# Kernel optimization log

Measured on AMD Instinct MI355X. Metric: run time of the kernel, lower is better.

The kernel has to match this reference:

```python
import jax, jax.numpy as jnp
import numpy as np

B, TX, TY, D, H = 8, 128, 128, 512, 512
LN_EPS = 1e-3  # keras LayerNormalization default epsilon


def setup_inputs() -> dict:
    key = jax.random.key(0)
    ks = jax.random.split(key, 6)
    scale = 1.0 / np.sqrt(D)
    return {
        "context": jax.random.normal(ks[0], (B, TX, D), jnp.float32),
        "x": jax.random.normal(ks[1], (B, TY, D), jnp.float32),
        "Wa": jax.random.normal(ks[2], (D, H), jnp.float32) * scale,
        "bWa": jnp.zeros((H,), jnp.float32),
        "Ua": jax.random.normal(ks[3], (D, H), jnp.float32) * scale,
        "bUa": jnp.zeros((H,), jnp.float32),
        "Va": jax.random.normal(ks[4], (H, 1), jnp.float32) * (1.0 / np.sqrt(H)),
        "bVa": jnp.zeros((1,), jnp.float32),
        "gamma": jnp.ones((D,), jnp.float32),
        "beta": jnp.zeros((D,), jnp.float32),
    }


def reference(context, x, Wa, bWa, Ua, bUa, Va, bVa, gamma, beta):
    # context: [B,Tx,D], x: [B,Ty,D]
    Wc = context @ Wa + bWa                      # [B,Tx,H]
    Ux = x @ Ua + bUa                            # [B,Ty,H]
    t = jnp.tanh(Wc[:, None, :, :] + Ux[:, :, None, :])  # [B,Ty,Tx,H]
    scores = jnp.einsum('btxh,h->btx', t, Va[:, 0]) + bVa[0]  # [B,Ty,Tx]
    attn = jax.nn.softmax(scores, axis=-1)
    cv = jnp.einsum('btx,bxd->btd', attn, context)  # [B,Ty,D]
    mean = jnp.mean(cv, axis=-1, keepdims=True)
    var = jnp.mean(jnp.square(cv - mean), axis=-1, keepdims=True)
    cv = (cv - mean) * jax.lax.rsqrt(var + LN_EPS) * gamma + beta
    return cv + x
```

## Files before the change

kernel.cpp:

```cpp
#include <hip/hip_runtime.h>


#define SCALE 2.8853900817779268f

typedef __attribute__((ext_vector_type(8))) short short8;
typedef float floatx4 __attribute__((ext_vector_type(4)));

__device__ __forceinline__ unsigned short f2bf(float f) {
  union { float f; unsigned u; } c{f};
  unsigned r = (c.u + 0x7FFFu + ((c.u >> 16) & 1u)) >> 16;
  return (unsigned short)r;
}

__global__ __launch_bounds__(256) void prep_transpose(
    const float* __restrict__ Wa, const float* __restrict__ Ua,
    unsigned short* __restrict__ WaT, unsigned short* __restrict__ UaT) {
  const int id = blockIdx.x;
  const float* __restrict__ W = (id & 64) ? Ua : Wa;
  unsigned short* __restrict__ WT = (id & 64) ? UaT : WaT;
  const int tile = id & 63;
  const int k0 = (tile >> 3) * 64;
  const int n0 = (tile & 7) * 64;
  __shared__ float tl[64][65];
  const int t = threadIdx.x;
  const int c = t & 63, r0 = t >> 6;
#pragma unroll
  for (int p = 0; p < 16; p++) {
    const int k = r0 + p * 4;
    tl[k][c] = W[(k0 + k) * 512 + n0 + c];
  }
  __syncthreads();
  const int nl = t >> 2, kc = (t & 3) * 16;
  unsigned short ov[16];
#pragma unroll
  for (int q = 0; q < 16; q++) ov[q] = f2bf(tl[kc + q][nl]);
  *(short8*)&WT[(size_t)(n0 + nl) * 512 + k0 + kc]     = *(short8*)&ov[0];
  *(short8*)&WT[(size_t)(n0 + nl) * 512 + k0 + kc + 8] = *(short8*)&ov[8];
}

__global__ __launch_bounds__(512) void gemm_mfma(
    const float* __restrict__ ctx, const float* __restrict__ xin,
    const unsigned short* __restrict__ WaT, const unsigned short* __restrict__ UaT,
    const float* __restrict__ bWa, const float* __restrict__ bUa,
    float* __restrict__ WcT, float* __restrict__ Ux) {
  const bool second = (blockIdx.z != 0);
  const float* __restrict__ A = second ? xin : ctx;
  const unsigned short* __restrict__ BT = second ? UaT : WaT;
  const int m0 = blockIdx.x * 64, n0 = blockIdx.y * 64;

  __shared__ __align__(16) unsigned short As[64 * 32];
  __shared__ __align__(16) unsigned short Bs[64 * 32];

  const int t = threadIdx.x;
  const bool isA = (t < 256);
  const int s = isA ? t : (t - 256);
  const int sl = s & 63, sub = s >> 6;
  const int rl = sub * 16 + (sl & 15);
  const int kl = (sl >> 4) * 8;

  const float* aptr = A + (size_t)(m0 + rl) * 512 + kl;
  const unsigned short* bptr = BT + (size_t)(n0 + rl) * 512 + kl;

  const int lane = t & 63, w = t >> 6;
  const int wrow = w & 1, wcol = w >> 1;

  floatx4 acc[2] = {};

  float4 a0, a1; short8 bv;
  if (isA) { a0 = *(const float4*)(aptr); a1 = *(const float4*)(aptr + 4); }
  else     { bv = *(const short8*)(bptr); }

  for (int kt = 0; kt < 512; kt += 32) {
    if (isA) {
      short8 av;
      av[0] = (short)f2bf(a0.x); av[1] = (short)f2bf(a0.y);
      av[2] = (short)f2bf(a0.z); av[3] = (short)f2bf(a0.w);
      av[4] = (short)f2bf(a1.x); av[5] = (short)f2bf(a1.y);
      av[6] = (short)f2bf(a1.z); av[7] = (short)f2bf(a1.w);
      ((short8*)As)[s] = av;
    } else {
      ((short8*)Bs)[s] = bv;
    }
    __syncthreads();
    if (kt + 32 < 512) {
      if (isA) {
        a0 = *(const float4*)(aptr + kt + 32);
        a1 = *(const float4*)(aptr + kt + 36);
      } else {
        bv = *(const short8*)(bptr + kt + 32);
      }
    }
    short8 af[2], bf;
    af[0] = ((const short8*)As)[(wrow * 2 + 0) * 64 + lane];
    af[1] = ((const short8*)As)[(wrow * 2 + 1) * 64 + lane];
    bf    = ((const short8*)Bs)[wcol * 64 + lane];
#pragma unroll
    for (int i = 0; i < 2; i++)
      acc[i] = __builtin_amdgcn_mfma_f32_16x16x32_bf16(af[i], bf, acc[i], 0, 0, 0);
    __syncthreads();
  }

  const int quad = lane >> 4;
  const int h = n0 + wcol * 16 + (lane & 15);
  if (!second) {
    const float bias = bWa[h] + bUa[h];
#pragma unroll
    for (int i = 0; i < 2; i++) {
      const int mg0 = m0 + (wrow * 2 + i) * 16 + quad * 4;
      const int b = mg0 >> 7, tx0 = mg0 & 127;
      float4 o;
      o.x = (acc[i][0] + bias) * SCALE;
      o.y = (acc[i][1] + bias) * SCALE;
      o.z = (acc[i][2] + bias) * SCALE;
      o.w = (acc[i][3] + bias) * SCALE;
      *(float4*)&WcT[(size_t)b * 65536 + (size_t)h * 128 + tx0] = o;
    }
  } else {
#pragma unroll
    for (int i = 0; i < 2; i++) {
      const int mg0 = m0 + (wrow * 2 + i) * 16 + quad * 4;
#pragma unroll
      for (int r = 0; r < 4; r++)
        Ux[(size_t)(mg0 + r) * 512 + h] = acc[i][r] * SCALE;
    }
  }
}

__global__ __launch_bounds__(512) void attn3(
    const float* __restrict__ WcT, const float* __restrict__ Ux,
    const float* __restrict__ ctx, const float* __restrict__ xin,
    const float* __restrict__ Va,
    const float* __restrict__ gamma, const float* __restrict__ beta,
    float* __restrict__ out) {
  const int b = blockIdx.y;
  const int ty0 = blockIdx.x * 2;
  const int t = threadIdx.x;
  const int lane = t & 63, wv = t >> 6;

  __shared__ __align__(8) float2 s_ux[512];
  __shared__ float s_va[512];
  __shared__ float s_part[8][128];
  __shared__ __align__(8) float2 s_at[128];
  __shared__ float s_red[2][2][8];
  __shared__ float s_mv[2][2];

  {
    const float* uxb = Ux + (size_t)(b * 128 + ty0) * 512;
    for (int i = t; i < 1024; i += 512) {
      const int r = i >> 9, h = i & 511;
      ((float*)&s_ux[h])[r] = uxb[i];
    }
    s_va[t] = Va[t];
  }
  __syncthreads();

  const int tx = t & 127, hq = t >> 7;
  {
    const float* wp = WcT + (size_t)b * 65536 + (size_t)hq * 128 * 128 + tx;
    float a0 = 0.f, a1 = 0.f;
#pragma unroll 4
    for (int hh = 0; hh < 128; hh++) {
      const float w = wp[(size_t)hh * 128];
      const float2 u = s_ux[hq * 128 + hh];
      const float va = s_va[hq * 128 + hh];
      a0 = fmaf(va, __builtin_amdgcn_rcpf(1.0f + __builtin_amdgcn_exp2f(w + u.x)), a0);
      a1 = fmaf(va, __builtin_amdgcn_rcpf(1.0f + __builtin_amdgcn_exp2f(w + u.y)), a1);
    }
    s_part[hq * 2 + 0][tx] = a0;
    s_part[hq * 2 + 1][tx] = a1;
  }
  __syncthreads();

  if (wv < 2) {
    const int r = wv;
    float sA = -2.0f * (s_part[r][lane] + s_part[2 + r][lane] +
                        s_part[4 + r][lane] + s_part[6 + r][lane]);
    float sB = -2.0f * (s_part[r][lane + 64] + s_part[2 + r][lane + 64] +
                        s_part[4 + r][lane + 64] + s_part[6 + r][lane + 64]);
    float m = fmaxf(sA, sB);
#pragma unroll
    for (int off = 32; off; off >>= 1) m = fmaxf(m, __shfl_xor(m, off));
    const float eA = __expf(sA - m);
    const float eB = __expf(sB - m);
    float sm = eA + eB;
#pragma unroll
    for (int off = 32; off; off >>= 1) sm += __shfl_xor(sm, off);
    const float inv = __builtin_amdgcn_rcpf(sm);
    ((float*)&s_at[lane])[r] = eA * inv;
    ((float*)&s_at[lane + 64])[r] = eB * inv;
  }
  __syncthreads();

  const int d = t;
  float cv0 = 0.f, cv1 = 0.f;
  {
    const float* cp = ctx + (size_t)b * 65536 + d;
#pragma unroll 4
    for (int x = 0; x < 128; x++) {
      const float c = cp[(size_t)x * 512];
      const float2 at = s_at[x];
      cv0 = fmaf(at.x, c, cv0);
      cv1 = fmaf(at.y, c, cv1);
    }
  }

#pragma unroll
  for (int r = 0; r < 2; r++) {
    const float v = r ? cv1 : cv0;
    float sm = v, q = v * v;
#pragma unroll
    for (int off = 32; off; off >>= 1) {
      sm += __shfl_xor(sm, off);
      q += __shfl_xor(q, off);
    }
    if (lane == 0) { s_red[r][0][wv] = sm; s_red[r][1][wv] = q; }
  }
  __syncthreads();
  if (t < 2) {
    float sm = 0.f, q = 0.f;
#pragma unroll
    for (int i = 0; i < 8; i++) { sm += s_red[t][0][i]; q += s_red[t][1][i]; }
    const float mean = sm * (1.0f / 512.0f);
    const float var = q * (1.0f / 512.0f) - mean * mean;
    s_mv[t][0] = mean;
    s_mv[t][1] = __builtin_amdgcn_rsqf(var + 1e-3f);
  }
  __syncthreads();

  const float g = gamma[d], bb = beta[d];
#pragma unroll
  for (int r = 0; r < 2; r++) {
    const int row = b * 128 + ty0 + r;
    const float v = r ? cv1 : cv0;
    const float xv = xin[(size_t)row * 512 + d];
    out[(size_t)row * 512 + d] = (v - s_mv[r][0]) * s_mv[r][1] * g + bb + xv;
  }
}

extern "C" void kernel_launch(void* const* d_in, const int* in_sizes, int n_in,
                              void* d_out, int out_size, void* d_ws, size_t ws_size,
                              hipStream_t stream) {
  const float* ctx   = (const float*)d_in[0];
  const float* xin   = (const float*)d_in[1];
  const float* Wa    = (const float*)d_in[2];
  const float* bWa   = (const float*)d_in[3];
  const float* Ua    = (const float*)d_in[4];
  const float* bUa   = (const float*)d_in[5];
  const float* Va    = (const float*)d_in[6];
  const float* gamma = (const float*)d_in[8];
  const float* beta  = (const float*)d_in[9];
  float* out = (float*)d_out;

  char* ws = (char*)d_ws;
  float* WcT = (float*)ws;
  float* Ux  = (float*)(ws + (2u << 20));
  unsigned short* WaT = (unsigned short*)(ws + (4u << 20));
  unsigned short* UaT = (unsigned short*)(ws + (4u << 20) + (512u << 10));

  prep_transpose<<<128, 256, 0, stream>>>(Wa, Ua, WaT, UaT);
  gemm_mfma<<<dim3(16, 8, 2), 512, 0, stream>>>(ctx, xin, WaT, UaT, bWa, bUa, WcT, Ux);
  attn3<<<dim3(64, 8), 512, 0, stream>>>(WcT, Ux, ctx, xin, Va, gamma, beta, out);
}
```

Before: 117.7 us.

## Fuse weight transpose into GEMM and process four query rows per attention block

The separate prep_transpose kernel is removed. The GEMM now loads fp32 weights directly with strided per-k reads, converts them to bf16 in registers, and uses a 64-wide k step per stage. The attention kernel moves to 1024-thread blocks that each handle four query rows, so every WcT and context load is reused across more rows. The cost is one fewer launch, traded against strided uncoalesced-ish weight loads, fewer blocks (256) for the attention kernel, and idle threads in the context-reduction phase.

```diff
diff --git a/kernel.cpp b/kernel.cpp
--- a/kernel.cpp
+++ b/kernel.cpp
@@ -12,102 +12,76 @@
   return (unsigned short)r;
 }
 
-__global__ __launch_bounds__(256) void prep_transpose(
+__global__ __launch_bounds__(512) void gemm_all(
+    const float* __restrict__ ctx, const float* __restrict__ xin,
     const float* __restrict__ Wa, const float* __restrict__ Ua,
-    unsigned short* __restrict__ WaT, unsigned short* __restrict__ UaT) {
-  const int id = blockIdx.x;
-  const float* __restrict__ W = (id & 64) ? Ua : Wa;
-  unsigned short* __restrict__ WT = (id & 64) ? UaT : WaT;
-  const int tile = id & 63;
-  const int k0 = (tile >> 3) * 64;
-  const int n0 = (tile & 7) * 64;
-  __shared__ float tl[64][65];
-  const int t = threadIdx.x;
-  const int c = t & 63, r0 = t >> 6;
-#pragma unroll
-  for (int p = 0; p < 16; p++) {
-    const int k = r0 + p * 4;
-    tl[k][c] = W[(k0 + k) * 512 + n0 + c];
-  }
-  __syncthreads();
-  const int nl = t >> 2, kc = (t & 3) * 16;
-  unsigned short ov[16];
-#pragma unroll
-  for (int q = 0; q < 16; q++) ov[q] = f2bf(tl[kc + q][nl]);
-  *(short8*)&WT[(size_t)(n0 + nl) * 512 + k0 + kc]     = *(short8*)&ov[0];
-  *(short8*)&WT[(size_t)(n0 + nl) * 512 + k0 + kc + 8] = *(short8*)&ov[8];
-}
-
-__global__ __launch_bounds__(512) void gemm_mfma(
-    const float* __restrict__ ctx, const float* __restrict__ xin,
-    const unsigned short* __restrict__ WaT, const unsigned short* __restrict__ UaT,
     const float* __restrict__ bWa, const float* __restrict__ bUa,
     float* __restrict__ WcT, float* __restrict__ Ux) {
   const bool second = (blockIdx.z != 0);
   const float* __restrict__ A = second ? xin : ctx;
-  const unsigned short* __restrict__ BT = second ? UaT : WaT;
+  const float* __restrict__ W = second ? Ua : Wa;
   const int m0 = blockIdx.x * 64, n0 = blockIdx.y * 64;
 
-  __shared__ __align__(16) unsigned short As[64 * 32];
-  __shared__ __align__(16) unsigned short Bs[64 * 32];
+  __shared__ __align__(16) unsigned short As[512 * 8];
+  __shared__ __align__(16) unsigned short Bs[512 * 8];
 
   const int t = threadIdx.x;
-  const bool isA = (t < 256);
-  const int s = isA ? t : (t - 256);
-  const int sl = s & 63, sub = s >> 6;
-  const int rl = sub * 16 + (sl & 15);
-  const int kl = (sl >> 4) * 8;
-
-  const float* aptr = A + (size_t)(m0 + rl) * 512 + kl;
-  const unsigned short* bptr = BT + (size_t)(n0 + rl) * 512 + kl;
-
-  const int lane = t & 63, w = t >> 6;
-  const int wrow = w & 1, wcol = w >> 1;
-
+  const int lane = t & 63, wv = t >> 6;
+
+  const int skst = t >> 8;
+  const int ssub = (t >> 6) & 3;
+  const int srow = ssub * 16 + (lane & 15);
+  const int sk   = skst * 32 + (lane >> 4) * 8;
+
+  const float* aptr = A + (size_t)(m0 + srow) * 512 + sk;
+  const float* wptr = W + (size_t)sk * 512 + n0 + srow;
+
+  const int wrow = wv & 3, wcol = wv >> 2;
   floatx4 acc[2] = {};
 
-  float4 a0, a1; short8 bv;
-  if (isA) { a0 = *(const float4*)(aptr); a1 = *(const float4*)(aptr + 4); }
-  else     { bv = *(const short8*)(bptr); }
-
-  for (int kt = 0; kt < 512; kt += 32) {
-    if (isA) {
-      short8 av;
-      av[0] = (short)f2bf(a0.x); av[1] = (short)f2bf(a0.y);
-      av[2] = (short)f2bf(a0.z); av[3] = (short)f2bf(a0.w);
-      av[4] = (short)f2bf(a1.x); av[5] = (short)f2bf(a1.y);
-      av[6] = (short)f2bf(a1.z); av[7] = (short)f2bf(a1.w);
-      ((short8*)As)[s] = av;
-    } else {
-      ((short8*)Bs)[s] = bv;
-    }
+  float4 a0 = *(const float4*)(aptr);
+  float4 a1 = *(const float4*)(aptr + 4);
+  float bw[8];
+#pragma unroll
+  for (int j = 0; j < 8; j++) bw[j] = wptr[(size_t)j * 512];
+
+  for (int kt = 0; kt < 512; kt += 64) {
+    short8 av, bv;
+    av[0] = (short)f2bf(a0.x); av[1] = (short)f2bf(a0.y);
+    av[2] = (short)f2bf(a0.z); av[3] = (short)f2bf(a0.w);
+    av[4] = (short)f2bf(a1.x); av[5] = (short)f2bf(a1.y);
+    av[6] = (short)f2bf(a1.z); av[7] = (short)f2bf(a1.w);
+#pragma unroll
+    for (int j = 0; j < 8; j++) bv[j] = (short)f2bf(bw[j]);
+    ((short8*)As)[t] = av;
+    ((short8*)Bs)[t] = bv;
     __syncthreads();
-    if (kt + 32 < 512) {
-      if (isA) {
-        a0 = *(const float4*)(aptr + kt + 32);
-        a1 = *(const float4*)(aptr + kt + 36);
-      } else {
-        bv = *(const short8*)(bptr + kt + 32);
-      }
-    }
-    short8 af[2], bf;
-    af[0] = ((const short8*)As)[(wrow * 2 + 0) * 64 + lane];
-    af[1] = ((const short8*)As)[(wrow * 2 + 1) * 64 + lane];
-    bf    = ((const short8*)Bs)[wcol * 64 + lane];
-#pragma unroll
-    for (int i = 0; i < 2; i++)
-      acc[i] = __builtin_amdgcn_mfma_f32_16x16x32_bf16(af[i], bf, acc[i], 0, 0, 0);
+    if (kt + 64 < 512) {
+      a0 = *(const float4*)(aptr + kt + 64);
+      a1 = *(const float4*)(aptr + kt + 68);
+      const float* wp2 = wptr + (size_t)(kt + 64) * 512;
+#pragma unroll
+      for (int j = 0; j < 8; j++) bw[j] = wp2[(size_t)j * 512];
+    }
+#pragma unroll
+    for (int ks = 0; ks < 2; ks++) {
+      const short8 af  = ((const short8*)As)[ks * 256 + wrow * 64 + lane];
+      const short8 bf0 = ((const short8*)Bs)[ks * 256 + (wcol * 2 + 0) * 64 + lane];
+      const short8 bf1 = ((const short8*)Bs)[ks * 256 + (wcol * 2 + 1) * 64 + lane];
+      acc[0] = __builtin_amdgcn_mfma_f32_16x16x32_bf16(af, bf0, acc[0], 0, 0, 0);
+      acc[1] = __builtin_amdgcn_mfma_f32_16x16x32_bf16(af, bf1, acc[1], 0, 0, 0);
+    }
     __syncthreads();
   }
 
   const int quad = lane >> 4;
-  const int h = n0 + wcol * 16 + (lane & 15);
+  const int mg0 = m0 + wrow * 16 + quad * 4;
   if (!second) {
-    const float bias = bWa[h] + bUa[h];
+    const int b = mg0 >> 7, tx0 = mg0 & 127;
 #pragma unroll
     for (int i = 0; i < 2; i++) {
-      const int mg0 = m0 + (wrow * 2 + i) * 16 + quad * 4;
-      const int b = mg0 >> 7, tx0 = mg0 & 127;
+      const int h = n0 + wcol * 32 + i * 16 + (lane & 15);
+      const float bias = bWa[h] + bUa[h];
       float4 o;
       o.x = (acc[i][0] + bias) * SCALE;
       o.y = (acc[i][1] + bias) * SCALE;
@@ -118,7 +92,7 @@
   } else {
 #pragma unroll
     for (int i = 0; i < 2; i++) {
-      const int mg0 = m0 + (wrow * 2 + i) * 16 + quad * 4;
+      const int h = n0 + wcol * 32 + i * 16 + (lane & 15);
 #pragma unroll
       for (int r = 0; r < 4; r++)
         Ux[(size_t)(mg0 + r) * 512 + h] = acc[i][r] * SCALE;
@@ -126,57 +100,64 @@
   }
 }
 
-__global__ __launch_bounds__(512) void attn3(
+__global__ __launch_bounds__(1024) void attn4(
     const float* __restrict__ WcT, const float* __restrict__ Ux,
     const float* __restrict__ ctx, const float* __restrict__ xin,
     const float* __restrict__ Va,
     const float* __restrict__ gamma, const float* __restrict__ beta,
     float* __restrict__ out) {
-  const int b = blockIdx.y;
-  const int ty0 = blockIdx.x * 2;
+  const int b = blockIdx.x >> 5;
+  const int ty0 = (blockIdx.x & 31) * 4;
   const int t = threadIdx.x;
   const int lane = t & 63, wv = t >> 6;
 
-  __shared__ __align__(8) float2 s_ux[512];
+  __shared__ __align__(16) float4 s_ux[512];
   __shared__ float s_va[512];
-  __shared__ float s_part[8][128];
-  __shared__ __align__(8) float2 s_at[128];
-  __shared__ float s_red[2][2][8];
-  __shared__ float s_mv[2][2];
+  __shared__ float s_part[32][128];
+  __shared__ __align__(16) float4 s_at[128];
+  __shared__ float s_red[4][2][8];
+  __shared__ float s_mv[4][2];
 
   {
     const float* uxb = Ux + (size_t)(b * 128 + ty0) * 512;
-    for (int i = t; i < 1024; i += 512) {
+    for (int i = t; i < 2048; i += 1024) {
       const int r = i >> 9, h = i & 511;
       ((float*)&s_ux[h])[r] = uxb[i];
     }
-    s_va[t] = Va[t];
+    if (t < 512) s_va[t] = Va[t];
   }
   __syncthreads();
 
   const int tx = t & 127, hq = t >> 7;
   {
-    const float* wp = WcT + (size_t)b * 65536 + (size_t)hq * 128 * 128 + tx;
-    float a0 = 0.f, a1 = 0.f;
+    const float* wp = WcT + (size_t)b * 65536 + (size_t)hq * 8192 + tx;
+    float a0 = 0.f, a1 = 0.f, a2 = 0.f, a3 = 0.f;
 #pragma unroll 4
-    for (int hh = 0; hh < 128; hh++) {
+    for (int hh = 0; hh < 64; hh++) {
       const float w = wp[(size_t)hh * 128];
-      const float2 u = s_ux[hq * 128 + hh];
-      const float va = s_va[hq * 128 + hh];
+      const float4 u = s_ux[hq * 64 + hh];
+      const float va = s_va[hq * 64 + hh];
       a0 = fmaf(va, __builtin_amdgcn_rcpf(1.0f + __builtin_amdgcn_exp2f(w + u.x)), a0);
       a1 = fmaf(va, __builtin_amdgcn_rcpf(1.0f + __builtin_amdgcn_exp2f(w + u.y)), a1);
-    }
-    s_part[hq * 2 + 0][tx] = a0;
-    s_part[hq * 2 + 1][tx] = a1;
-  }
-  __syncthreads();
-
-  if (wv < 2) {
+      a2 = fmaf(va, __builtin_amdgcn_rcpf(1.0f + __builtin_amdgcn_exp2f(w + u.z)), a2);
+      a3 = fmaf(va, __builtin_amdgcn_rcpf(1.0f + __builtin_amdgcn_exp2f(w + u.w)), a3);
+    }
+    s_part[hq * 4 + 0][tx] = a0;
+    s_part[hq * 4 + 1][tx] = a1;
+    s_part[hq * 4 + 2][tx] = a2;
+    s_part[hq * 4 + 3][tx] = a3;
+  }
+  __syncthreads();
+
+  if (wv < 4) {
     const int r = wv;
-    float sA = -2.0f * (s_part[r][lane] + s_part[2 + r][lane] +
-                        s_part[4 + r][lane] + s_part[6 + r][lane]);
-    float sB = -2.0f * (s_part[r][lane + 64] + s_part[2 + r][lane + 64] +
-                        s_part[4 + r][lane + 64] + s_part[6 + r][lane + 64]);
+    float sA = 0.f, sB = 0.f;
+#pragma unroll
+    for (int q = 0; q < 8; q++) {
+      sA += s_part[q * 4 + r][lane];
+      sB += s_part[q * 4 + r][lane + 64];
+    }
+    sA *= -2.0f; sB *= -2.0f;
     float m = fmaxf(sA, sB);
 #pragma unroll
     for (int off = 32; off; off >>= 1) m = fmaxf(m, __shfl_xor(m, off));
@@ -191,32 +172,31 @@
   }
   __syncthreads();
 
-  const int d = t;
-  float cv0 = 0.f, cv1 = 0.f;
-  {
-    const float* cp = ctx + (size_t)b * 65536 + d;
+  float cv[4] = {0.f, 0.f, 0.f, 0.f};
+  if (t < 512) {
+    const float* cp = ctx + (size_t)b * 65536 + t;
 #pragma unroll 4
     for (int x = 0; x < 128; x++) {
       const float c = cp[(size_t)x * 512];
-      const float2 at = s_at[x];
-      cv0 = fmaf(at.x, c, cv0);
-      cv1 = fmaf(at.y, c, cv1);
-    }
-  }
-
-#pragma unroll
-  for (int r = 0; r < 2; r++) {
-    const float v = r ? cv1 : cv0;
-    float sm = v, q = v * v;
-#pragma unroll
-    for (int off = 32; off; off >>= 1) {
-      sm += __shfl_xor(sm, off);
-      q += __shfl_xor(q, off);
-    }
-    if (lane == 0) { s_red[r][0][wv] = sm; s_red[r][1][wv] = q; }
-  }
-  __syncthreads();
-  if (t < 2) {
+      const float4 at = s_at[x];
+      cv[0] = fmaf(at.x, c, cv[0]);
+      cv[1] = fmaf(at.y, c, cv[1]);
+      cv[2] = fmaf(at.z, c, cv[2]);
+      cv[3] = fmaf(at.w, c, cv[3]);
+    }
+#pragma unroll
+    for (int r = 0; r < 4; r++) {
+      float sm = cv[r], q = cv[r] * cv[r];
+#pragma unroll
+      for (int off = 32; off; off >>= 1) {
+        sm += __shfl_xor(sm, off);
+        q += __shfl_xor(q, off);
+      }
+      if (lane == 0) { s_red[r][0][wv] = sm; s_red[r][1][wv] = q; }
+    }
+  }
+  __syncthreads();
+  if (t < 4) {
     float sm = 0.f, q = 0.f;
 #pragma unroll
     for (int i = 0; i < 8; i++) { sm += s_red[t][0][i]; q += s_red[t][1][i]; }
@@ -227,13 +207,14 @@
   }
   __syncthreads();
 
-  const float g = gamma[d], bb = beta[d];
-#pragma unroll
-  for (int r = 0; r < 2; r++) {
-    const int row = b * 128 + ty0 + r;
-    const float v = r ? cv1 : cv0;
-    const float xv = xin[(size_t)row * 512 + d];
-    out[(size_t)row * 512 + d] = (v - s_mv[r][0]) * s_mv[r][1] * g + bb + xv;
+  if (t < 512) {
+    const float g = gamma[t], bb = beta[t];
+#pragma unroll
+    for (int r = 0; r < 4; r++) {
+      const int row = b * 128 + ty0 + r;
+      const float xv = xin[(size_t)row * 512 + t];
+      out[(size_t)row * 512 + t] = (cv[r] - s_mv[r][0]) * s_mv[r][1] * g + bb + xv;
+    }
   }
 }
 
@@ -254,10 +235,7 @@
   char* ws = (char*)d_ws;
   float* WcT = (float*)ws;
   float* Ux  = (float*)(ws + (2u << 20));
-  unsigned short* WaT = (unsigned short*)(ws + (4u << 20));
-  unsigned short* UaT = (unsigned short*)(ws + (4u << 20) + (512u << 10));
-
-  prep_transpose<<<128, 256, 0, stream>>>(Wa, Ua, WaT, UaT);
-  gemm_mfma<<<dim3(16, 8, 2), 512, 0, stream>>>(ctx, xin, WaT, UaT, bWa, bUa, WcT, Ux);
-  attn3<<<dim3(64, 8), 512, 0, stream>>>(WcT, Ux, ctx, xin, Va, gamma, beta, out);
-}
+
+  gemm_all<<<dim3(16, 8, 2), 512, 0, stream>>>(ctx, xin, Wa, Ua, bWa, bUa, WcT, Ux);
+  attn4<<<256, 1024, 0, stream>>>(WcT, Ux, ctx, xin, Va, gamma, beta, out);
+}
```

Result: faster. 109.2 us (-7.2%).
